# Kernel tuning notes

Hardware: AMD Instinct MI355X
Metric: run time of the kernel (lower is better)

Reference implementation:

```python
import jax, jax.numpy as jnp
import numpy as np

L, B, Q, D = 6, 2, 300, 256  # levels, batch, num queries, embed dim


def setup_inputs() -> dict:
    key = jax.random.key(0)
    ks = jax.random.split(key, 20)
    s = 1.0 / np.sqrt(D)
    s2 = 1.0 / np.sqrt(2 * D)
    inp = {
        "hs": jax.random.normal(ks[0], (L, B, Q, D), jnp.float32),
        # per-level proj_q / proj_k (Linear(D, D) cloned L times)
        "Wq": jax.random.uniform(ks[1], (L, D, D), jnp.float32, -s, s),
        "bq": jax.random.uniform(ks[2], (L, D), jnp.float32, -s, s),
        "Wk": jax.random.uniform(ks[3], (L, D, D), jnp.float32, -s, s),
        "bk": jax.random.uniform(ks[4], (L, D), jnp.float32, -s, s),
        # final subject/object projections on hs[-1]
        "Wsub": jax.random.uniform(ks[5], (D, D), jnp.float32, -s, s),
        "bsub": jax.random.uniform(ks[6], (D,), jnp.float32, -s, s),
        "Wobj": jax.random.uniform(ks[7], (D, D), jnp.float32, -s, s),
        "bobj": jax.random.uniform(ks[8], (D,), jnp.float32, -s, s),
        # gate: Linear(2D, 1)
        "Wg": jax.random.uniform(ks[9], (2 * D, 1), jnp.float32, -s2, s2),
        "bg": jax.random.uniform(ks[10], (1,), jnp.float32, -s2, s2),
        # MLPHEAD: 2D -> D -> D -> 1
        "W1": jax.random.uniform(ks[11], (2 * D, D), jnp.float32, -s2, s2),
        "b1": jax.random.uniform(ks[12], (D,), jnp.float32, -s2, s2),
        "W2": jax.random.uniform(ks[13], (D, D), jnp.float32, -s, s),
        "b2": jax.random.uniform(ks[14], (D,), jnp.float32, -s, s),
        "W3": jax.random.uniform(ks[15], (D, 1), jnp.float32, -s, s),
        "b3": jax.random.uniform(ks[16], (1,), jnp.float32, -s, s),
    }
    return inp


def reference(hs, Wq, bq, Wk, bk, Wsub, bsub, Wobj, bobj, Wg, bg, W1, b1, W2, b2, W3, b3):
    l, b, q, d = hs.shape
    # per-level projections: [L, B, Q, D]
    Qs = jnp.einsum('lbqd,lde->lbqe', hs, Wq) + bq[:, None, None, :]
    Ks = jnp.einsum('lbqd,lde->lbqe', hs, Wk) + bk[:, None, None, :]
    # extra (L+1)-th level from final sub/obj projections of hs[-1]
    sub = hs[-1] @ Wsub + bsub  # [B, Q, D]
    obj = hs[-1] @ Wobj + bobj
    Q_all = jnp.concatenate([Qs, sub[None]], axis=0)  # [L+1, B, Q, D]
    K_all = jnp.concatenate([Ks, obj[None]], axis=0)
    # gate logit for pair (i, j) at level m = wa.q_m[i] + wb.k_m[j] + bg,
    # identical math to sigmoid(Linear(cat([q_i, k_j]))) without materializing
    # the [B, Q, Q, L+1, 2D] broadcast tensor.
    wa, wb = Wg[:d, 0], Wg[d:, 0]
    gq = jnp.einsum('lbqd,d->lbq', Q_all, wa)  # [L+1, B, Q]
    gk = jnp.einsum('lbqd,d->lbq', K_all, wb)
    gate = jax.nn.sigmoid(gq[:, :, :, None] + gk[:, :, None, :] + bg[0])  # [L+1, B, Qi, Qj]
    # gated sum over levels; query half depends on i, key half on j
    out_q = jnp.einsum('lbij,lbid->bijd', gate, Q_all)  # [B, Q, Q, D]
    out_k = jnp.einsum('lbij,lbjd->bijd', gate, K_all)
    gated = jnp.concatenate([out_q, out_k], axis=-1)  # [B, Q, Q, 2D]
    # rel predictor MLP: 2D -> D -> D -> 1
    x = jax.nn.relu(gated @ W1 + b1)
    x = jax.nn.relu(x @ W2 + b2)
    pred = (x @ W3 + b3)[..., 0]  # [B, Q, Q]
    pred_rel = jnp.broadcast_to(pred[None], (l,) + pred.shape)  # [L, B, Q, Q]
    return pred_rel
```

## Files before the change

### kernel.cpp

```cpp
#include <hip/hip_runtime.h>


typedef _Float16 half8 __attribute__((ext_vector_type(8)));
typedef _Float16 half4v __attribute__((ext_vector_type(4)));
typedef float floatx4 __attribute__((ext_vector_type(4)));

#define MFMA16(a, b, c) __builtin_amdgcn_mfma_f32_16x16x32_f16((a), (b), (c), 0, 0, 0)

__global__ __launch_bounds__(256) void k_wprep(
    const float* __restrict__ Wq, const float* __restrict__ Wk,
    const float* __restrict__ Wsub, const float* __restrict__ Wobj,
    const float* __restrict__ W1, const float* __restrict__ W2,
    _Float16* __restrict__ WT)
{
    int eid = blockIdx.x * 256 + threadIdx.x;
    int mat = eid >> 13;
    int rem = eid & 8191;
    int tileid = rem >> 6;
    int lane = rem & 63;
    const float* src;
    if      (mat < 6)  src = Wq + mat * 65536;
    else if (mat < 12) src = Wk + (mat - 6) * 65536;
    else if (mat == 12) src = Wsub;
    else if (mat == 13) src = Wobj;
    else if (mat == 14) src = W1;
    else if (mat == 15) src = W1 + 65536;
    else               src = W2;
    int nb = tileid >> 3, kb = tileid & 7;
    int n = nb * 16 + (lane & 15);
    int k = kb * 32 + (lane >> 4) * 8;
    half8 h;
    #pragma unroll
    for (int j = 0; j < 8; ++j) h[j] = (_Float16)src[(k + j) * 256 + n];
    *(half8*)(WT + mat * 65536 + tileid * 512 + lane * 8) = h;
}

__global__ __launch_bounds__(256) void k_projpq(
    const float* __restrict__ hs, const _Float16* __restrict__ WT,
    const float* __restrict__ bq, const float* __restrict__ bk,
    const float* __restrict__ bsub, const float* __restrict__ bobj,
    const float* __restrict__ Wg,
    _Float16* __restrict__ PQt, _Float16* __restrict__ PKt,
    float* __restrict__ g_ws)
{
    __shared__ __align__(16) _Float16 Ah[32][264];
    __shared__ __align__(16) _Float16 X[32][264];

    int bid = blockIdx.x;
    int s = bid / 10, rt = bid - s * 10;
    int m0 = rt * 32;
    int qk = s & 1, rr = s >> 1;
    int l = rr % 7, b = rr / 7;
    int hs_l = (l < 6) ? l : 5;
    const float* src = hs + (hs_l * 2 + b) * 76800;
    int projmat = (l < 6) ? (qk * 6 + l) : (12 + qk);
    const _Float16* WprojT = WT + projmat * 65536;
    const _Float16* W1hT   = WT + (14 + qk) * 65536;
    const float* bias = (l < 6) ? ((qk ? bk : bq) + l * 256) : (qk ? bobj : bsub);
    _Float16* dstP = qk ? PKt : PQt;
    const float* wvec = Wg + qk * 256;
    float* gdst = g_ws + qk * 4200 + (l * 2 + b) * 300;

    int t = threadIdx.x, lane = t & 63, wv = t >> 6;
    int mr = lane & 15, hf = lane >> 4;

    {
        int row = t >> 3, qt = t & 7;
        int m = m0 + row; if (m > 299) m = 299;
        const float* p = src + m * 256 + qt * 32;
        #pragma unroll
        for (int i = 0; i < 8; ++i) {
            float4 v = *(const float4*)(p + 4 * i);
            half4v h;
            h[0] = (_Float16)v.x; h[1] = (_Float16)v.y;
            h[2] = (_Float16)v.z; h[3] = (_Float16)v.w;
            *(half4v*)&Ah[row][qt * 32 + 4 * i] = h;
        }
    }
    __syncthreads();

    floatx4 acc[4][2];
    #pragma unroll
    for (int i = 0; i < 4; ++i)
        #pragma unroll
        for (int j = 0; j < 2; ++j) acc[i][j] = floatx4{0.f, 0.f, 0.f, 0.f};
    for (int ks = 0; ks < 8; ++ks) {
        half8 bfr[2];
        #pragma unroll
        for (int nt = 0; nt < 2; ++nt)
            bfr[nt] = *(const half8*)&Ah[nt * 16 + mr][ks * 32 + hf * 8];
        #pragma unroll
        for (int mt = 0; mt < 4; ++mt) {
            half8 afr = *(const half8*)(WprojT + (((wv * 4 + mt) * 8 + ks) << 9) + lane * 8);
            #pragma unroll
            for (int nt = 0; nt < 2; ++nt)
                acc[mt][nt] = MFMA16(afr, bfr[nt], acc[mt][nt]);
        }
    }

    #pragma unroll
    for (int mt = 0; mt < 4; ++mt) {
        int n0 = wv * 64 + mt * 16 + hf * 4;
        float4 bb = *(const float4*)&bias[n0];
        float bv[4] = {bb.x, bb.y, bb.z, bb.w};
        #pragma unroll
        for (int nt = 0; nt < 2; ++nt) {
            int r = nt * 16 + mr;
            half4v h;
            #pragma unroll
            for (int u = 0; u < 4; ++u) h[u] = (_Float16)(acc[mt][nt][u] + bv[u]);
            *(half4v*)&X[r][n0] = h;
        }
    }
    __syncthreads();

    {
        int row = t >> 3, qt = t & 7;
        float sum = 0.f;
        #pragma unroll
        for (int i = 0; i < 32; i += 8) {
            half8 xv = *(const half8*)&X[row][qt * 32 + i];
            const float* wp = wvec + qt * 32 + i;
            float4 w0 = *(const float4*)wp;
            float4 w1 = *(const float4*)(wp + 4);
            sum += (float)xv[0] * w0.x + (float)xv[1] * w0.y
                 + (float)xv[2] * w0.z + (float)xv[3] * w0.w
                 + (float)xv[4] * w1.x + (float)xv[5] * w1.y
                 + (float)xv[6] * w1.z + (float)xv[7] * w1.w;
        }
        sum += __shfl_xor(sum, 1);
        sum += __shfl_xor(sum, 2);
        sum += __shfl_xor(sum, 4);
        int m = m0 + row;
        if (qt == 0 && m < 300) gdst[m] = sum;
    }

    floatx4 acc2[4][2];
    #pragma unroll
    for (int i = 0; i < 4; ++i)
        #pragma unroll
        for (int j = 0; j < 2; ++j) acc2[i][j] = floatx4{0.f, 0.f, 0.f, 0.f};
    for (int ks = 0; ks < 8; ++ks) {
        half8 bfr[2];
        #pragma unroll
        for (int nt = 0; nt < 2; ++nt)
            bfr[nt] = *(const half8*)&X[nt * 16 + mr][ks * 32 + hf * 8];
        #pragma unroll
        for (int mt = 0; mt < 4; ++mt) {
            half8 afr = *(const half8*)(W1hT + (((wv * 4 + mt) * 8 + ks) << 9) + lane * 8);
            #pragma unroll
            for (int nt = 0; nt < 2; ++nt)
                acc2[mt][nt] = MFMA16(afr, bfr[nt], acc2[mt][nt]);
        }
    }

    #pragma unroll
    for (int mt = 0; mt < 4; ++mt) {
        int n0 = wv * 64 + mt * 16 + hf * 4;
        #pragma unroll
        for (int nt = 0; nt < 2; ++nt) {
            int r = nt * 16 + mr;
            half4v h;
            #pragma unroll
            for (int u = 0; u < 4; ++u) h[u] = (_Float16)acc2[mt][nt][u];
            *(half4v*)&Ah[r][n0] = h;
        }
    }
    __syncthreads();

    for (int z = 0; z < 4; ++z) {
        int task = z * 256 + t;
        int it4 = task >> 8, n = task & 255;
        int it = rt * 4 + it4;
        if (it < 38) {
            half8 h;
            #pragma unroll
            for (int io = 0; io < 8; ++io) h[io] = Ah[it4 * 8 + io][n];
            *(half8*)(dstP + ((size_t)(b * 38 + it) * 256 + n) * 56 + l * 8) = h;
        }
    }
}

__global__ __launch_bounds__(256, 4) void k_fused(
    const _Float16* __restrict__ PQt, const _Float16* __restrict__ PKt,
    const float* __restrict__ g_ws, const float* __restrict__ b1,
    const _Float16* __restrict__ W2T, const float* __restrict__ b2,
    const float* __restrict__ W3, const float* __restrict__ b3,
    const float* __restrict__ bg, float* __restrict__ out)
{
    union SM {
        _Float16 Pt[256][72];
        _Float16 X[64][264];
    };
    __shared__ __align__(16) SM sm;
    __shared__ float gate[7][64];

    int t = threadIdx.x, lane = t & 63, wv = t >> 6;
    int mr = lane & 15, hf = lane >> 4;
    int bid = blockIdx.x;
    int b = bid / 1444, rem = bid - b * 1444;
    int it = rem / 38, jt = rem - it * 38;
    int i0 = it * 8, j0 = jt * 8;

    float bg0 = bg[0];
    for (int task = t; task < 448; task += 256) {
        int l = task >> 6, row = task & 63;
        int i = i0 + (row >> 3); if (i > 299) i = 299;
        int j = j0 + (row & 7);  if (j > 299) j = 299;
        float z = g_ws[l * 600 + b * 300 + i] + g_ws[4200 + l * 600 + b * 300 + j] + bg0;
        gate[l][row] = 1.0f / (1.0f + __expf(-z));
    }

    floatx4 acc1[4][4];
    #pragma unroll
    for (int i = 0; i < 4; ++i)
        #pragma unroll
        for (int j = 0; j < 4; ++j) acc1[i][j] = floatx4{0.f, 0.f, 0.f, 0.f};

    #pragma unroll
    for (int pass = 0; pass < 2; ++pass) {
        const _Float16* src = pass ? PKt : PQt;
        int tb = pass ? jt : it;
        const _Float16* gp = src + ((size_t)(b * 38 + tb) * 256 + t) * 56;
        __syncthreads();
        #pragma unroll
        for (int l = 0; l < 7; ++l)
            *(half8*)&sm.Pt[t][l * 8] = *(const half8*)(gp + l * 8);
        *(half8*)&sm.Pt[t][56] = half8{};
        __syncthreads();

        #pragma unroll
        for (int ktl = 0; ktl < 2; ++ktl) {
            int l = ktl * 4 + hf;
            half8 bfr[4];
            #pragma unroll
            for (int nt = 0; nt < 4; ++nt) {
                int r = nt * 16 + mr;
                float g = (l < 7) ? gate[l][r] : 0.f;
                _Float16 gh = (_Float16)g;
                const _Float16 hz = (_Float16)0.f;
                half8 f = {};
                if (pass == 0) {
                    f[nt * 2]     = (mr < 8)  ? gh : hz;
                    f[nt * 2 + 1] = (mr >= 8) ? gh : hz;
                } else {
                    #pragma unroll
                    for (int j = 0; j < 8; ++j)
                        f[j] = (j == (mr & 7)) ? gh : hz;
                }
                bfr[nt] = f;
            }
            #pragma unroll
            for (int mt = 0; mt < 4; ++mt) {
                half8 afr = *(const half8*)&sm.Pt[wv * 64 + mt * 16 + mr][ktl * 32 + hf * 8];
                #pragma unroll
                for (int nt = 0; nt < 4; ++nt)
                    acc1[mt][nt] = MFMA16(afr, bfr[nt], acc1[mt][nt]);
            }
        }
    }
    __syncthreads();

    #pragma unroll
    for (int mt = 0; mt < 4; ++mt) {
        int n0 = wv * 64 + mt * 16 + hf * 4;
        float4 bb = *(const float4*)&b1[n0];
        float bv[4] = {bb.x, bb.y, bb.z, bb.w};
        #pragma unroll
        for (int nt = 0; nt < 4; ++nt) {
            int r = nt * 16 + mr;
            half4v h;
            #pragma unroll
            for (int u = 0; u < 4; ++u) {
                float v = acc1[mt][nt][u] + bv[u];
                h[u] = (_Float16)(v > 0.f ? v : 0.f);
            }
            *(half4v*)&sm.X[r][n0] = h;
        }
    }
    __syncthreads();

    floatx4 acc2[4][4];
    #pragma unroll
    for (int i = 0; i < 4; ++i)
        #pragma unroll
        for (int j = 0; j < 4; ++j) acc2[i][j] = floatx4{0.f, 0.f, 0.f, 0.f};
    for (int s = 0; s < 8; ++s) {
        half8 bfr[4];
        #pragma unroll
        for (int nt = 0; nt < 4; ++nt)
            bfr[nt] = *(const half8*)&sm.X[nt * 16 + mr][s * 32 + hf * 8];
        #pragma unroll
        for (int mt = 0; mt < 4; ++mt) {
            half8 afr = *(const half8*)(W2T + (((wv * 4 + mt) * 8 + s) << 9) + lane * 8);
            #pragma unroll
            for (int nt = 0; nt < 4; ++nt)
                acc2[mt][nt] = MFMA16(afr, bfr[nt], acc2[mt][nt]);
        }
    }

    {
        float* red = &gate[0][0];
        float p[4] = {0.f, 0.f, 0.f, 0.f};
        #pragma unroll
        for (int mt = 0; mt < 4; ++mt) {
            int n0 = wv * 64 + mt * 16 + hf * 4;
            float4 bb = *(const float4*)&b2[n0];
            float4 w3 = *(const float4*)&W3[n0];
            float bv[4] = {bb.x, bb.y, bb.z, bb.w};
            float wv3[4] = {w3.x, w3.y, w3.z, w3.w};
            #pragma unroll
            for (int nt = 0; nt < 4; ++nt)
                #pragma unroll
                for (int u = 0; u < 4; ++u) {
                    float v = acc2[mt][nt][u] + bv[u];
                    v = v > 0.f ? v : 0.f;
                    p[nt] += v * wv3[u];
                }
        }
        #pragma unroll
        for (int nt = 0; nt < 4; ++nt) {
            p[nt] += __shfl_xor(p[nt], 16);
            p[nt] += __shfl_xor(p[nt], 32);
        }
        if (hf == 0) {
            #pragma unroll
            for (int nt = 0; nt < 4; ++nt)
                red[wv * 64 + nt * 16 + mr] = p[nt];
        }
        __syncthreads();
        if (t < 64) {
            float pred = red[t] + red[64 + t] + red[128 + t] + red[192 + t] + b3[0];
            int i = i0 + (t >> 3), j = j0 + (t & 7);
            if (i < 300 && j < 300) {
                int base = b * 90000 + i * 300 + j;
                #pragma unroll
                for (int lo = 0; lo < 6; ++lo) out[lo * 180000 + base] = pred;
            }
        }
    }
}

extern "C" void kernel_launch(void* const* d_in, const int* in_sizes, int n_in,
                              void* d_out, int out_size, void* d_ws, size_t ws_size,
                              hipStream_t stream) {
    (void)in_sizes; (void)n_in; (void)out_size; (void)ws_size;
    const float* hs   = (const float*)d_in[0];
    const float* Wq   = (const float*)d_in[1];
    const float* bq   = (const float*)d_in[2];
    const float* Wk   = (const float*)d_in[3];
    const float* bk   = (const float*)d_in[4];
    const float* Wsub = (const float*)d_in[5];
    const float* bsub = (const float*)d_in[6];
    const float* Wobj = (const float*)d_in[7];
    const float* bobj = (const float*)d_in[8];
    const float* Wg   = (const float*)d_in[9];
    const float* bg   = (const float*)d_in[10];
    const float* W1   = (const float*)d_in[11];
    const float* b1   = (const float*)d_in[12];
    const float* W2   = (const float*)d_in[13];
    const float* b2   = (const float*)d_in[14];
    const float* W3   = (const float*)d_in[15];
    const float* b3   = (const float*)d_in[16];

    char* ws = (char*)d_ws;
    float* g_ws   = (float*)ws;
    _Float16* WT  = (_Float16*)(ws + 33600);
    _Float16* PQt = WT + 17 * 65536;
    _Float16* PKt = PQt + 1089536;

    k_wprep<<<544, 256, 0, stream>>>(Wq, Wk, Wsub, Wobj, W1, W2, WT);
    k_projpq<<<280, 256, 0, stream>>>(hs, WT, bq, bk, bsub, bobj, Wg,
                                      PQt, PKt, g_ws);
    k_fused<<<2888, 256, 0, stream>>>(PQt, PKt, g_ws, b1, WT + 16 * 65536,
                                      b2, W3, b3, bg, (float*)d_out);
}
```

Before: 147.8 us.

## Merge three kernels into one persistent cooperative kernel with grid syncs

```diff
diff --git a/kernel.cpp b/kernel.cpp
--- a/kernel.cpp
+++ b/kernel.cpp
@@ -1,4 +1,7 @@
 #include <hip/hip_runtime.h>
+#include <hip/hip_cooperative_groups.h>
+
+namespace cg = cooperative_groups;
 
 
 typedef _Float16 half8 __attribute__((ext_vector_type(8)));
@@ -7,335 +10,302 @@
 
 #define MFMA16(a, b, c) __builtin_amdgcn_mfma_f32_16x16x32_f16((a), (b), (c), 0, 0, 0)
 
-__global__ __launch_bounds__(256) void k_wprep(
-    const float* __restrict__ Wq, const float* __restrict__ Wk,
-    const float* __restrict__ Wsub, const float* __restrict__ Wobj,
-    const float* __restrict__ W1, const float* __restrict__ W2,
-    _Float16* __restrict__ WT)
+struct Params {
+    const float *hs, *Wq, *bq, *Wk, *bk, *Wsub, *bsub, *Wobj, *bobj, *Wg, *bg,
+                *W1, *b1, *W2, *b2, *W3, *b3;
+    _Float16 *WT, *PQt, *PKt;
+    float *g_ws, *out;
+};
+
+union MegaSM {
+    struct { _Float16 Ah[32][264]; _Float16 Xb[32][264]; } B;
+    struct {
+        union { _Float16 Pt[256][72]; _Float16 X[64][264]; } sm;
+        float gate[7][64];
+    } C;
+};
+
+__global__ __launch_bounds__(256, 4) void k_mega(Params p)
 {
-    int eid = blockIdx.x * 256 + threadIdx.x;
-    int mat = eid >> 13;
-    int rem = eid & 8191;
-    int tileid = rem >> 6;
-    int lane = rem & 63;
-    const float* src;
-    if      (mat < 6)  src = Wq + mat * 65536;
-    else if (mat < 12) src = Wk + (mat - 6) * 65536;
-    else if (mat == 12) src = Wsub;
-    else if (mat == 13) src = Wobj;
-    else if (mat == 14) src = W1;
-    else if (mat == 15) src = W1 + 65536;
-    else               src = W2;
-    int nb = tileid >> 3, kb = tileid & 7;
-    int n = nb * 16 + (lane & 15);
-    int k = kb * 32 + (lane >> 4) * 8;
-    half8 h;
-    #pragma unroll
-    for (int j = 0; j < 8; ++j) h[j] = (_Float16)src[(k + j) * 256 + n];
-    *(half8*)(WT + mat * 65536 + tileid * 512 + lane * 8) = h;
-}
-
-__global__ __launch_bounds__(256) void k_projpq(
-    const float* __restrict__ hs, const _Float16* __restrict__ WT,
-    const float* __restrict__ bq, const float* __restrict__ bk,
-    const float* __restrict__ bsub, const float* __restrict__ bobj,
-    const float* __restrict__ Wg,
-    _Float16* __restrict__ PQt, _Float16* __restrict__ PKt,
-    float* __restrict__ g_ws)
-{
-    __shared__ __align__(16) _Float16 Ah[32][264];
-    __shared__ __align__(16) _Float16 X[32][264];
-
-    int bid = blockIdx.x;
-    int s = bid / 10, rt = bid - s * 10;
-    int m0 = rt * 32;
-    int qk = s & 1, rr = s >> 1;
-    int l = rr % 7, b = rr / 7;
-    int hs_l = (l < 6) ? l : 5;
-    const float* src = hs + (hs_l * 2 + b) * 76800;
-    int projmat = (l < 6) ? (qk * 6 + l) : (12 + qk);
-    const _Float16* WprojT = WT + projmat * 65536;
-    const _Float16* W1hT   = WT + (14 + qk) * 65536;
-    const float* bias = (l < 6) ? ((qk ? bk : bq) + l * 256) : (qk ? bobj : bsub);
-    _Float16* dstP = qk ? PKt : PQt;
-    const float* wvec = Wg + qk * 256;
-    float* gdst = g_ws + qk * 4200 + (l * 2 + b) * 300;
-
+    __shared__ __align__(16) MegaSM S;
     int t = threadIdx.x, lane = t & 63, wv = t >> 6;
     int mr = lane & 15, hf = lane >> 4;
-
-    {
-        int row = t >> 3, qt = t & 7;
-        int m = m0 + row; if (m > 299) m = 299;
-        const float* p = src + m * 256 + qt * 32;
-        #pragma unroll
-        for (int i = 0; i < 8; ++i) {
-            float4 v = *(const float4*)(p + 4 * i);
+    int bid = blockIdx.x, nblk = gridDim.x;
+
+    for (int e0 = bid * 256; e0 < 139264; e0 += nblk * 256) {
+        int eid = e0 + t;
+        int mat = eid >> 13, rem = eid & 8191;
+        int tileid = rem >> 6, ln = rem & 63;
+        const float* src;
+        if      (mat < 6)  src = p.Wq + mat * 65536;
+        else if (mat < 12) src = p.Wk + (mat - 6) * 65536;
+        else if (mat == 12) src = p.Wsub;
+        else if (mat == 13) src = p.Wobj;
+        else if (mat == 14) src = p.W1;
+        else if (mat == 15) src = p.W1 + 65536;
+        else               src = p.W2;
+        int nb = tileid >> 3, kb = tileid & 7;
+        int n = nb * 16 + (ln & 15);
+        int k = kb * 32 + (ln >> 4) * 8;
+        half8 h;
+        #pragma unroll
+        for (int j = 0; j < 8; ++j) h[j] = (_Float16)src[(k + j) * 256 + n];
+        *(half8*)(p.WT + mat * 65536 + tileid * 512 + ln * 8) = h;
+    }
+    cg::this_grid().sync();
+
+    for (int u = bid; u < 532; u += nblk) {
+        __syncthreads();
+        int s = u / 19, rt = u - s * 19;
+        int m0 = rt * 16;
+        int qk = s & 1, rr = s >> 1;
+        int l = rr % 7, b = rr / 7;
+        int hs_l = (l < 6) ? l : 5;
+        const float* src = p.hs + (hs_l * 2 + b) * 76800;
+        int projmat = (l < 6) ? (qk * 6 + l) : (12 + qk);
+        const _Float16* WprojT = p.WT + projmat * 65536;
+        const _Float16* W1hT = p.WT + (14 + qk) * 65536;
+        const float* bias = (l < 6) ? ((qk ? p.bk : p.bq) + l * 256)
+                                    : (qk ? p.bobj : p.bsub);
+        _Float16* dstP = qk ? p.PKt : p.PQt;
+        const float* wvec = p.Wg + qk * 256;
+        float* gdst = p.g_ws + qk * 4200 + (l * 2 + b) * 300;
+
+        {
+            int row = t >> 4, qt = t & 15;
+            int m = m0 + row; if (m > 299) m = 299;
+            const float* pp = src + m * 256 + qt * 16;
+            #pragma unroll
+            for (int i = 0; i < 4; ++i) {
+                float4 v = *(const float4*)(pp + 4 * i);
+                half4v h;
+                h[0] = (_Float16)v.x; h[1] = (_Float16)v.y;
+                h[2] = (_Float16)v.z; h[3] = (_Float16)v.w;
+                *(half4v*)&S.B.Ah[row][qt * 16 + 4 * i] = h;
+            }
+        }
+        __syncthreads();
+
+        floatx4 acc[4];
+        #pragma unroll
+        for (int i = 0; i < 4; ++i) acc[i] = floatx4{0.f, 0.f, 0.f, 0.f};
+        for (int ks = 0; ks < 8; ++ks) {
+            half8 bfr = *(const half8*)&S.B.Ah[mr][ks * 32 + hf * 8];
+            #pragma unroll
+            for (int mt = 0; mt < 4; ++mt) {
+                half8 afr = *(const half8*)(WprojT + (((wv * 4 + mt) * 8 + ks) << 9) + lane * 8);
+                acc[mt] = MFMA16(afr, bfr, acc[mt]);
+            }
+        }
+        #pragma unroll
+        for (int mt = 0; mt < 4; ++mt) {
+            int n0 = wv * 64 + mt * 16 + hf * 4;
+            float4 bb = *(const float4*)&bias[n0];
+            float bv[4] = {bb.x, bb.y, bb.z, bb.w};
             half4v h;
-            h[0] = (_Float16)v.x; h[1] = (_Float16)v.y;
-            h[2] = (_Float16)v.z; h[3] = (_Float16)v.w;
-            *(half4v*)&Ah[row][qt * 32 + 4 * i] = h;
+            #pragma unroll
+            for (int u2 = 0; u2 < 4; ++u2) h[u2] = (_Float16)(acc[mt][u2] + bv[u2]);
+            *(half4v*)&S.B.Xb[mr][n0] = h;
+        }
+        __syncthreads();
+
+        {
+            int row = t >> 4, qt = t & 15;
+            half8 x0 = *(const half8*)&S.B.Xb[row][qt * 16];
+            half8 x1 = *(const half8*)&S.B.Xb[row][qt * 16 + 8];
+            const float* wp = wvec + qt * 16;
+            float sum = 0.f;
+            #pragma unroll
+            for (int i = 0; i < 8; ++i) sum += (float)x0[i] * wp[i];
+            #pragma unroll
+            for (int i = 0; i < 8; ++i) sum += (float)x1[i] * wp[8 + i];
+            sum += __shfl_xor(sum, 1);
+            sum += __shfl_xor(sum, 2);
+            sum += __shfl_xor(sum, 4);
+            sum += __shfl_xor(sum, 8);
+            int m = m0 + row;
+            if (qt == 0 && m < 300) gdst[m] = sum;
+        }
+
+        floatx4 acc2[4];
+        #pragma unroll
+        for (int i = 0; i < 4; ++i) acc2[i] = floatx4{0.f, 0.f, 0.f, 0.f};
+        for (int ks = 0; ks < 8; ++ks) {
+            half8 bfr = *(const half8*)&S.B.Xb[mr][ks * 32 + hf * 8];
+            #pragma unroll
+            for (int mt = 0; mt < 4; ++mt) {
+                half8 afr = *(const half8*)(W1hT + (((wv * 4 + mt) * 8 + ks) << 9) + lane * 8);
+                acc2[mt] = MFMA16(afr, bfr, acc2[mt]);
+            }
+        }
+        #pragma unroll
+        for (int mt = 0; mt < 4; ++mt) {
+            int n0 = wv * 64 + mt * 16 + hf * 4;
+            half4v h;
+            #pragma unroll
+            for (int u2 = 0; u2 < 4; ++u2) h[u2] = (_Float16)acc2[mt][u2];
+            *(half4v*)&S.B.Ah[mr][n0] = h;
+        }
+        __syncthreads();
+
+        #pragma unroll
+        for (int z = 0; z < 2; ++z) {
+            int task = z * 256 + t;
+            int it2 = task >> 8, n = task & 255;
+            int it = rt * 2 + it2;
+            if (it < 38) {
+                half8 h;
+                #pragma unroll
+                for (int io = 0; io < 8; ++io) h[io] = S.B.Ah[it2 * 8 + io][n];
+                *(half8*)(dstP + ((size_t)(b * 38 + it) * 256 + n) * 56 + l * 8) = h;
+            }
         }
     }
-    __syncthreads();
-
-    floatx4 acc[4][2];
-    #pragma unroll
-    for (int i = 0; i < 4; ++i)
-        #pragma unroll
-        for (int j = 0; j < 2; ++j) acc[i][j] = floatx4{0.f, 0.f, 0.f, 0.f};
-    for (int ks = 0; ks < 8; ++ks) {
-        half8 bfr[2];
-        #pragma unroll
-        for (int nt = 0; nt < 2; ++nt)
-            bfr[nt] = *(const half8*)&Ah[nt * 16 + mr][ks * 32 + hf * 8];
+    cg::this_grid().sync();
+
+    const _Float16* W2T = p.WT + 16 * 65536;
+    for (int tile = bid; tile < 2888; tile += nblk) {
+        __syncthreads();
+        int b = tile / 1444, rem = tile - b * 1444;
+        int it = rem / 38, jt = rem - it * 38;
+        int i0 = it * 8, j0 = jt * 8;
+
+        float bg0 = p.bg[0];
+        for (int task = t; task < 448; task += 256) {
+            int l = task >> 6, row = task & 63;
+            int i = i0 + (row >> 3); if (i > 299) i = 299;
+            int j = j0 + (row & 7);  if (j > 299) j = 299;
+            float z = p.g_ws[l * 600 + b * 300 + i]
+                    + p.g_ws[4200 + l * 600 + b * 300 + j] + bg0;
+            S.C.gate[l][row] = 1.0f / (1.0f + __expf(-z));
+        }
+
+        floatx4 acc1[4][4];
+        #pragma unroll
+        for (int i = 0; i < 4; ++i)
+            #pragma unroll
+            for (int j = 0; j < 4; ++j) acc1[i][j] = floatx4{0.f, 0.f, 0.f, 0.f};
+
+        #pragma unroll
+        for (int pass = 0; pass < 2; ++pass) {
+            const _Float16* srcP = pass ? p.PKt : p.PQt;
+            int tb = pass ? jt : it;
+            const _Float16* gp = srcP + ((size_t)(b * 38 + tb) * 256 + t) * 56;
+            __syncthreads();
+            #pragma unroll
+            for (int l = 0; l < 7; ++l)
+                *(half8*)&S.C.sm.Pt[t][l * 8] = *(const half8*)(gp + l * 8);
+            *(half8*)&S.C.sm.Pt[t][56] = half8{};
+            __syncthreads();
+
+            #pragma unroll
+            for (int ktl = 0; ktl < 2; ++ktl) {
+                int l = ktl * 4 + hf;
+                half8 bfr[4];
+                #pragma unroll
+                for (int nt = 0; nt < 4; ++nt) {
+                    int r = nt * 16 + mr;
+                    float g = (l < 7) ? S.C.gate[l][r] : 0.f;
+                    _Float16 gh = (_Float16)g;
+                    const _Float16 hz = (_Float16)0.f;
+                    half8 f = {};
+                    if (pass == 0) {
+                        f[nt * 2]     = (mr < 8)  ? gh : hz;
+                        f[nt * 2 + 1] = (mr >= 8) ? gh : hz;
+                    } else {
+                        #pragma unroll
+                        for (int j = 0; j < 8; ++j)
+                            f[j] = (j == (mr & 7)) ? gh : hz;
+                    }
+                    bfr[nt] = f;
+                }
+                #pragma unroll
+                for (int mt = 0; mt < 4; ++mt) {
+                    half8 afr = *(const half8*)&S.C.sm.Pt[wv * 64 + mt * 16 + mr][ktl * 32 + hf * 8];
+                    #pragma unroll
+                    for (int nt = 0; nt < 4; ++nt)
+                        acc1[mt][nt] = MFMA16(afr, bfr[nt], acc1[mt][nt]);
+                }
+            }
+        }
+        __syncthreads();
+
         #pragma unroll
         for (int mt = 0; mt < 4; ++mt) {
-            half8 afr = *(const half8*)(WprojT + (((wv * 4 + mt) * 8 + ks) << 9) + lane * 8);
-            #pragma unroll
-            for (int nt = 0; nt < 2; ++nt)
-                acc[mt][nt] = MFMA16(afr, bfr[nt], acc[mt][nt]);
-        }
-    }
-
-    #pragma unroll
-    for (int mt = 0; mt < 4; ++mt) {
-        int n0 = wv * 64 + mt * 16 + hf * 4;
-        float4 bb = *(const float4*)&bias[n0];
-        float bv[4] = {bb.x, bb.y, bb.z, bb.w};
-        #pragma unroll
-        for (int nt = 0; nt < 2; ++nt) {
-            int r = nt * 16 + mr;
-            half4v h;
-            #pragma unroll
-            for (int u = 0; u < 4; ++u) h[u] = (_Float16)(acc[mt][nt][u] + bv[u]);
-            *(half4v*)&X[r][n0] = h;
-        }
-    }
-    __syncthreads();
-
-    {
-        int row = t >> 3, qt = t & 7;
-        float sum = 0.f;
-        #pragma unroll
-        for (int i = 0; i < 32; i += 8) {
-            half8 xv = *(const half8*)&X[row][qt * 32 + i];
-            const float* wp = wvec + qt * 32 + i;
-            float4 w0 = *(const float4*)wp;
-            float4 w1 = *(const float4*)(wp + 4);
-            sum += (float)xv[0] * w0.x + (float)xv[1] * w0.y
-                 + (float)xv[2] * w0.z + (float)xv[3] * w0.w
-                 + (float)xv[4] * w1.x + (float)xv[5] * w1.y
-                 + (float)xv[6] * w1.z + (float)xv[7] * w1.w;
-        }
-        sum += __shfl_xor(sum, 1);
-        sum += __shfl_xor(sum, 2);
-        sum += __shfl_xor(sum, 4);
-        int m = m0 + row;
-        if (qt == 0 && m < 300) gdst[m] = sum;
-    }
-
-    floatx4 acc2[4][2];
-    #pragma unroll
-    for (int i = 0; i < 4; ++i)
-        #pragma unroll
-        for (int j = 0; j < 2; ++j) acc2[i][j] = floatx4{0.f, 0.f, 0.f, 0.f};
-    for (int ks = 0; ks < 8; ++ks) {
-        half8 bfr[2];
-        #pragma unroll
-        for (int nt = 0; nt < 2; ++nt)
-            bfr[nt] = *(const half8*)&X[nt * 16 + mr][ks * 32 + hf * 8];
-        #pragma unroll
-        for (int mt = 0; mt < 4; ++mt) {
-            half8 afr = *(const half8*)(W1hT + (((wv * 4 + mt) * 8 + ks) << 9) + lane * 8);
-            #pragma unroll
-            for (int nt = 0; nt < 2; ++nt)
-                acc2[mt][nt] = MFMA16(afr, bfr[nt], acc2[mt][nt]);
-        }
-    }
-
-    #pragma unroll
-    for (int mt = 0; mt < 4; ++mt) {
-        int n0 = wv * 64 + mt * 16 + hf * 4;
-        #pragma unroll
-        for (int nt = 0; nt < 2; ++nt) {
-            int r = nt * 16 + mr;
-            half4v h;
-            #pragma unroll
-            for (int u = 0; u < 4; ++u) h[u] = (_Float16)acc2[mt][nt][u];
-            *(half4v*)&Ah[r][n0] = h;
-        }
-    }
-    __syncthreads();
-
-    for (int z = 0; z < 4; ++z) {
-        int task = z * 256 + t;
-        int it4 = task >> 8, n = task & 255;
-        int it = rt * 4 + it4;
-        if (it < 38) {
-            half8 h;
-            #pragma unroll
-            for (int io = 0; io < 8; ++io) h[io] = Ah[it4 * 8 + io][n];
-            *(half8*)(dstP + ((size_t)(b * 38 + it) * 256 + n) * 56 + l * 8) = h;
-        }
-    }
-}
-
-__global__ __launch_bounds__(256, 4) void k_fused(
-    const _Float16* __restrict__ PQt, const _Float16* __restrict__ PKt,
-    const float* __restrict__ g_ws, const float* __restrict__ b1,
-    const _Float16* __restrict__ W2T, const float* __restrict__ b2,
-    const float* __restrict__ W3, const float* __restrict__ b3,
-    const float* __restrict__ bg, float* __restrict__ out)
-{
-    union SM {
-        _Float16 Pt[256][72];
-        _Float16 X[64][264];
-    };
-    __shared__ __align__(16) SM sm;
-    __shared__ float gate[7][64];
-
-    int t = threadIdx.x, lane = t & 63, wv = t >> 6;
-    int mr = lane & 15, hf = lane >> 4;
-    int bid = blockIdx.x;
-    int b = bid / 1444, rem = bid - b * 1444;
-    int it = rem / 38, jt = rem - it * 38;
-    int i0 = it * 8, j0 = jt * 8;
-
-    float bg0 = bg[0];
-    for (int task = t; task < 448; task += 256) {
-        int l = task >> 6, row = task & 63;
-        int i = i0 + (row >> 3); if (i > 299) i = 299;
-        int j = j0 + (row & 7);  if (j > 299) j = 299;
-        float z = g_ws[l * 600 + b * 300 + i] + g_ws[4200 + l * 600 + b * 300 + j] + bg0;
-        gate[l][row] = 1.0f / (1.0f + __expf(-z));
-    }
-
-    floatx4 acc1[4][4];
-    #pragma unroll
-    for (int i = 0; i < 4; ++i)
-        #pragma unroll
-        for (int j = 0; j < 4; ++j) acc1[i][j] = floatx4{0.f, 0.f, 0.f, 0.f};
-
-    #pragma unroll
-    for (int pass = 0; pass < 2; ++pass) {
-        const _Float16* src = pass ? PKt : PQt;
-        int tb = pass ? jt : it;
-        const _Float16* gp = src + ((size_t)(b * 38 + tb) * 256 + t) * 56;
-        __syncthreads();
-        #pragma unroll
-        for (int l = 0; l < 7; ++l)
-            *(half8*)&sm.Pt[t][l * 8] = *(const half8*)(gp + l * 8);
-        *(half8*)&sm.Pt[t][56] = half8{};
-        __syncthreads();
-
-        #pragma unroll
-        for (int ktl = 0; ktl < 2; ++ktl) {
-            int l = ktl * 4 + hf;
-            half8 bfr[4];
+            int n0 = wv * 64 + mt * 16 + hf * 4;
+            float4 bb = *(const float4*)&p.b1[n0];
+            float bv[4] = {bb.x, bb.y, bb.z, bb.w};
             #pragma unroll
             for (int nt = 0; nt < 4; ++nt) {
                 int r = nt * 16 + mr;
-                float g = (l < 7) ? gate[l][r] : 0.f;
-                _Float16 gh = (_Float16)g;
-                const _Float16 hz = (_Float16)0.f;
-                half8 f = {};
-                if (pass == 0) {
-                    f[nt * 2]     = (mr < 8)  ? gh : hz;
-                    f[nt * 2 + 1] = (mr >= 8) ? gh : hz;
-                } else {
+                half4v h;
+                #pragma unroll
+                for (int u2 = 0; u2 < 4; ++u2) {
+                    float v = acc1[mt][nt][u2] + bv[u2];
+                    h[u2] = (_Float16)(v > 0.f ? v : 0.f);
+                }
+                *(half4v*)&S.C.sm.X[r][n0] = h;
+            }
+        }
+        __syncthreads();
+
+        floatx4 acc2[4][4];
+        #pragma unroll
+        for (int i = 0; i < 4; ++i)
+            #pragma unroll
+            for (int j = 0; j < 4; ++j) acc2[i][j] = floatx4{0.f, 0.f, 0.f, 0.f};
+        for (int s2 = 0; s2 < 8; ++s2) {
+            half8 bfr[4];
+            #pragma unroll
+            for (int nt = 0; nt < 4; ++nt)
+                bfr[nt] = *(const half8*)&S.C.sm.X[nt * 16 + mr][s2 * 32 + hf * 8];
+            #pragma unroll
+            for (int mt = 0; mt < 4; ++mt) {
+                half8 afr = *(const half8*)(W2T + (((wv * 4 + mt) * 8 + s2) << 9) + lane * 8);
+                #pragma unroll
+                for (int nt = 0; nt < 4; ++nt)
+                    acc2[mt][nt] = MFMA16(afr, bfr[nt], acc2[mt][nt]);
+            }
+        }
+
+        {
+            float* red = &S.C.gate[0][0];
+            float pr[4] = {0.f, 0.f, 0.f, 0.f};
+            #pragma unroll
+            for (int mt = 0; mt < 4; ++mt) {
+                int n0 = wv * 64 + mt * 16 + hf * 4;
+                float4 bb = *(const float4*)&p.b2[n0];
+                float4 w3 = *(const float4*)&p.W3[n0];
+                float bv[4] = {bb.x, bb.y, bb.z, bb.w};
+                float wv3[4] = {w3.x, w3.y, w3.z, w3.w};
+                #pragma unroll
+                for (int nt = 0; nt < 4; ++nt)
                     #pragma unroll
-                    for (int j = 0; j < 8; ++j)
-                        f[j] = (j == (mr & 7)) ? gh : hz;
+                    for (int u2 = 0; u2 < 4; ++u2) {
+                        float v = acc2[mt][nt][u2] + bv[u2];
+                        v = v > 0.f ? v : 0.f;
+                        pr[nt] += v * wv3[u2];
+                    }
+            }
+            #pragma unroll
+            for (int nt = 0; nt < 4; ++nt) {
+                pr[nt] += __shfl_xor(pr[nt], 16);
+                pr[nt] += __shfl_xor(pr[nt], 32);
+            }
+            if (hf == 0) {
+                #pragma unroll
+                for (int nt = 0; nt < 4; ++nt)
+                    red[wv * 64 + nt * 16 + mr] = pr[nt];
+            }
+            __syncthreads();
+            if (t < 64) {
+                float pred = red[t] + red[64 + t] + red[128 + t] + red[192 + t] + p.b3[0];
+                int i = i0 + (t >> 3), j = j0 + (t & 7);
+                if (i < 300 && j < 300) {
+                    int base = b * 90000 + i * 300 + j;
+                    #pragma unroll
+                    for (int lo = 0; lo < 6; ++lo) p.out[lo * 180000 + base] = pred;
                 }
-                bfr[nt] = f;
-            }
-            #pragma unroll
-            for (int mt = 0; mt < 4; ++mt) {
-                half8 afr = *(const half8*)&sm.Pt[wv * 64 + mt * 16 + mr][ktl * 32 + hf * 8];
-                #pragma unroll
-                for (int nt = 0; nt < 4; ++nt)
-                    acc1[mt][nt] = MFMA16(afr, bfr[nt], acc1[mt][nt]);
-            }
-        }
-    }
-    __syncthreads();
-
-    #pragma unroll
-    for (int mt = 0; mt < 4; ++mt) {
-        int n0 = wv * 64 + mt * 16 + hf * 4;
-        float4 bb = *(const float4*)&b1[n0];
-        float bv[4] = {bb.x, bb.y, bb.z, bb.w};
-        #pragma unroll
-        for (int nt = 0; nt < 4; ++nt) {
-            int r = nt * 16 + mr;
-            half4v h;
-            #pragma unroll
-            for (int u = 0; u < 4; ++u) {
-                float v = acc1[mt][nt][u] + bv[u];
-                h[u] = (_Float16)(v > 0.f ? v : 0.f);
-            }
-            *(half4v*)&sm.X[r][n0] = h;
-        }
-    }
-    __syncthreads();
-
-    floatx4 acc2[4][4];
-    #pragma unroll
-    for (int i = 0; i < 4; ++i)
-        #pragma unroll
-        for (int j = 0; j < 4; ++j) acc2[i][j] = floatx4{0.f, 0.f, 0.f, 0.f};
-    for (int s = 0; s < 8; ++s) {
-        half8 bfr[4];
-        #pragma unroll
-        for (int nt = 0; nt < 4; ++nt)
-            bfr[nt] = *(const half8*)&sm.X[nt * 16 + mr][s * 32 + hf * 8];
-        #pragma unroll
-        for (int mt = 0; mt < 4; ++mt) {
-            half8 afr = *(const half8*)(W2T + (((wv * 4 + mt) * 8 + s) << 9) + lane * 8);
-            #pragma unroll
-            for (int nt = 0; nt < 4; ++nt)
-                acc2[mt][nt] = MFMA16(afr, bfr[nt], acc2[mt][nt]);
-        }
-    }
-
-    {
-        float* red = &gate[0][0];
-        float p[4] = {0.f, 0.f, 0.f, 0.f};
-        #pragma unroll
-        for (int mt = 0; mt < 4; ++mt) {
-            int n0 = wv * 64 + mt * 16 + hf * 4;
-            float4 bb = *(const float4*)&b2[n0];
-            float4 w3 = *(const float4*)&W3[n0];
-            float bv[4] = {bb.x, bb.y, bb.z, bb.w};
-            float wv3[4] = {w3.x, w3.y, w3.z, w3.w};
-            #pragma unroll
-            for (int nt = 0; nt < 4; ++nt)
-                #pragma unroll
-                for (int u = 0; u < 4; ++u) {
-                    float v = acc2[mt][nt][u] + bv[u];
-                    v = v > 0.f ? v : 0.f;
-                    p[nt] += v * wv3[u];
-                }
-        }
-        #pragma unroll
-        for (int nt = 0; nt < 4; ++nt) {
-            p[nt] += __shfl_xor(p[nt], 16);
-            p[nt] += __shfl_xor(p[nt], 32);
-        }
-        if (hf == 0) {
-            #pragma unroll
-            for (int nt = 0; nt < 4; ++nt)
-                red[wv * 64 + nt * 16 + mr] = p[nt];
-        }
-        __syncthreads();
-        if (t < 64) {
-            float pred = red[t] + red[64 + t] + red[128 + t] + red[192 + t] + b3[0];
-            int i = i0 + (t >> 3), j = j0 + (t & 7);
-            if (i < 300 && j < 300) {
-                int base = b * 90000 + i * 300 + j;
-                #pragma unroll
-                for (int lo = 0; lo < 6; ++lo) out[lo * 180000 + base] = pred;
             }
         }
     }
@@ -345,33 +315,38 @@
                               void* d_out, int out_size, void* d_ws, size_t ws_size,
                               hipStream_t stream) {
     (void)in_sizes; (void)n_in; (void)out_size; (void)ws_size;
-    const float* hs   = (const float*)d_in[0];
-    const float* Wq   = (const float*)d_in[1];
-    const float* bq   = (const float*)d_in[2];
-    const float* Wk   = (const float*)d_in[3];
-    const float* bk   = (const float*)d_in[4];
-    const float* Wsub = (const float*)d_in[5];
-    const float* bsub = (const float*)d_in[6];
-    const float* Wobj = (const float*)d_in[7];
-    const float* bobj = (const float*)d_in[8];
-    const float* Wg   = (const float*)d_in[9];
-    const float* bg   = (const float*)d_in[10];
-    const float* W1   = (const float*)d_in[11];
-    const float* b1   = (const float*)d_in[12];
-    const float* W2   = (const float*)d_in[13];
-    const float* b2   = (const float*)d_in[14];
-    const float* W3   = (const float*)d_in[15];
-    const float* b3   = (const float*)d_in[16];
-
     char* ws = (char*)d_ws;
     float* g_ws   = (float*)ws;
     _Float16* WT  = (_Float16*)(ws + 33600);
     _Float16* PQt = WT + 17 * 65536;
     _Float16* PKt = PQt + 1089536;
 
-    k_wprep<<<544, 256, 0, stream>>>(Wq, Wk, Wsub, Wobj, W1, W2, WT);
-    k_projpq<<<280, 256, 0, stream>>>(hs, WT, bq, bk, bsub, bobj, Wg,
-                                      PQt, PKt, g_ws);
-    k_fused<<<2888, 256, 0, stream>>>(PQt, PKt, g_ws, b1, WT + 16 * 65536,
-                                      b2, W3, b3, bg, (float*)d_out);
+    Params prm;
+    prm.hs   = (const float*)d_in[0];
+    prm.Wq   = (const float*)d_in[1];
+    prm.bq   = (const float*)d_in[2];
+    prm.Wk   = (const float*)d_in[3];
+    prm.bk   = (const float*)d_in[4];
+    prm.Wsub = (const float*)d_in[5];
+    prm.bsub = (const float*)d_in[6];
+    prm.Wobj = (const float*)d_in[7];
+    prm.bobj = (const float*)d_in[8];
+    prm.Wg   = (const float*)d_in[9];
+    prm.bg   = (const float*)d_in[10];
+    prm.W1   = (const float*)d_in[11];
+    prm.b1   = (const float*)d_in[12];
+    prm.W2   = (const float*)d_in[13];
+    prm.b2   = (const float*)d_in[14];
+    prm.W3   = (const float*)d_in[15];
+    prm.b3   = (const float*)d_in[16];
+    prm.WT = WT; prm.PQt = PQt; prm.PKt = PKt;
+    prm.g_ws = g_ws; prm.out = (float*)d_out;
+
+    int nb = 0;
+    hipOccupancyMaxActiveBlocksPerMultiprocessor(&nb, k_mega, 256, 0);
+    if (nb < 1) nb = 1;
+    if (nb > 4) nb = 4;
+    dim3 grid(nb * 256), block(256);
+    void* args[] = { &prm };
+    hipLaunchCooperativeKernel((void*)k_mega, grid, block, args, 0, stream);
 }
```

Measured after the change: 412.0 us. 2.79x slower.
